# Performance work log

Hardware: AMD Instinct MI355X
Metric: run time of the kernel (lower is better)

The kernel has to match this reference:

```python
import jax, jax.numpy as jnp
import numpy as np

ROUTING_ITERS = 3


def _squash(x, axis=-1):
    # sum_sq/(1+sum_sq) * x/sqrt(sum_sq), faithful to the torch squash
    sum_sq = jnp.sum(x * x, axis=axis, keepdims=True)
    return sum_sq / (1.0 + sum_sq) * x / jnp.sqrt(sum_sq)


def setup_inputs() -> dict:
    key = jax.random.key(0)
    k1, k2 = jax.random.split(key)
    B, I, O, Din, Dout = 256, 1152, 10, 8, 16
    x = jax.random.normal(k1, (B, I, Din), dtype=jnp.float32)
    W = jax.random.normal(k2, (I, O, Din, Dout), dtype=jnp.float32)
    return {"x": x, "W": W}


def reference(x, W):
    # x: [B, I, Din], W: [I, O, Din, Dout]
    I, O, Din, Dout = W.shape
    # u_hat = x @ W per (capsule_in, capsule_out): [B, I, O, Dout]
    u_hat = jnp.einsum('bid,iode->bioe', x, W)
    b = jnp.zeros((I, O), dtype=x.dtype)  # coupling logits, shared over batch
    v = None
    for _ in range(ROUTING_ITERS):
        c = jax.nn.softmax(b, axis=1)                    # softmax over out capsules
        s = jnp.einsum('bioe,io->boe', u_hat, c)         # weighted sum over in caps
        v = _squash(s, axis=-1)                          # [B, O, Dout]
        # agreement, averaged over batch (torch does .mean(dim=0))
        agree = jnp.einsum('bioe,boe->bio', u_hat, v).mean(axis=0)  # [I, O]
        b = b + agree
    # torch returns v.squeeze(1).transpose(2,3) -> [B, O, Dout, 1]
    return v[..., None]
```

## Files before the change

### kernel.cpp

```cpp
#include <hip/hip_runtime.h>
#include <math.h>

#define B    256
#define I    1152
#define O    10
#define DIN  8
#define DOUT 16
#define OE   160
#define XROW 9216
#define WROW 1280
#define PSPLIT 72
#define CHUNK  16
#define SI     8

typedef __attribute__((ext_vector_type(8))) short short8;
typedef __attribute__((ext_vector_type(4))) float floatx4;

__device__ __forceinline__ unsigned short f2bf(float f) {
    unsigned u = __builtin_bit_cast(unsigned, f);
    u += 0x7fffu + ((u >> 16) & 1u);
    return (unsigned short)(u >> 16);
}
__device__ __forceinline__ float bf2f(unsigned short h) {
    unsigned u = ((unsigned)h) << 16;
    return __builtin_bit_cast(float, u);
}

__global__ __launch_bounds__(256) void xsplit_kernel(
    const float* __restrict__ x,
    unsigned short* __restrict__ xh, unsigned short* __restrict__ xl)
{
    int g = blockIdx.x * 256 + threadIdx.x;
    float4 v = ((const float4*)x)[g];
    ushort4 h, l;
    h.x = f2bf(v.x); l.x = f2bf(v.x - bf2f(h.x));
    h.y = f2bf(v.y); l.y = f2bf(v.y - bf2f(h.y));
    h.z = f2bf(v.z); l.z = f2bf(v.z - bf2f(h.z));
    h.w = f2bf(v.w); l.w = f2bf(v.w - bf2f(h.w));
    ((ushort4*)xh)[g] = h;
    ((ushort4*)xl)[g] = l;
}

__global__ __launch_bounds__(256) void spart_mfma(
    const unsigned short* __restrict__ xh, const unsigned short* __restrict__ xl,
    const float* __restrict__ W, const float* __restrict__ c,
    float* __restrict__ sp, int first)
{
    __shared__ unsigned short Wh[80 * 64], Wl[80 * 64];
    __shared__ unsigned short Xh[128 * 64], Xl[128 * 64];

    int bid = blockIdx.x;
    int ic  = bid >> 2;
    int mb  = (bid >> 1) & 1;
    int nb  = bid & 1;
    int b0  = mb * 128;
    int oe0 = nb * 80;
    int o0  = nb * 5;
    int i0  = ic * CHUNK;

    int t    = threadIdx.x;
    int w    = t >> 6;
    int lane = t & 63;
    int l15  = lane & 15;
    int q    = lane >> 4;

    floatx4 acc[2][5];
#pragma unroll
    for (int mt = 0; mt < 2; ++mt)
#pragma unroll
        for (int nt = 0; nt < 5; ++nt) acc[mt][nt] = (floatx4)(0.f);

#pragma unroll
    for (int round = 0; round < CHUNK / SI; ++round) {
        int si0 = i0 + round * SI;
        if (round) __syncthreads();

#pragma unroll
        for (int r = 0; r < 3; ++r) {
            int p = t + 256 * r;
            if (p < 640) {
                int oeL = p % 80;
                int iL  = p / 80;
                int o   = o0 + (oeL >> 4);
                int e   = oeL & 15;
                const float* wp = W + (size_t)(si0 + iL) * WROW + o * (DIN * DOUT) + e;
                float cv = first ? 0.1f : c[(si0 + iL) * O + o];
                short8 hv, lv;
#pragma unroll
                for (int d = 0; d < 8; ++d) {
                    float wv = wp[d * DOUT] * cv;
                    unsigned short h = f2bf(wv);
                    hv[d] = (short)h;
                    lv[d] = (short)f2bf(wv - bf2f(h));
                }
                int off = oeL * 64 + ((iL ^ (oeL & 7)) << 3);
                *(short8*)(Wh + off) = hv;
                *(short8*)(Wl + off) = lv;
            }
        }
#pragma unroll
        for (int r = 0; r < 4; ++r) {
            int cg  = t + 256 * r;
            int row = cg >> 3;
            int ch  = cg & 7;
            size_t goff = (size_t)(b0 + row) * XROW + (size_t)si0 * 8 + (ch << 3);
            short8 vh = *(const short8*)(xh + goff);
            short8 vl = *(const short8*)(xl + goff);
            int off = row * 64 + ((ch ^ (row & 7)) << 3);
            *(short8*)(Xh + off) = vh;
            *(short8*)(Xl + off) = vl;
        }
        __syncthreads();

#pragma unroll
        for (int ks = 0; ks < 2; ++ks) {
            short8 ah[2], al[2];
#pragma unroll
            for (int mt = 0; mt < 2; ++mt) {
                int rm  = w * 32 + mt * 16 + l15;
                int off = rm * 64 + ((((ks << 2) + q) ^ (rm & 7)) << 3);
                ah[mt] = *(const short8*)(Xh + off);
                al[mt] = *(const short8*)(Xl + off);
            }
#pragma unroll
            for (int nt = 0; nt < 5; ++nt) {
                int rn  = nt * 16 + l15;
                int off = rn * 64 + ((((ks << 2) + q) ^ (rn & 7)) << 3);
                short8 bh = *(const short8*)(Wh + off);
                short8 bl = *(const short8*)(Wl + off);
#pragma unroll
                for (int mt = 0; mt < 2; ++mt) {
                    acc[mt][nt] = __builtin_amdgcn_mfma_f32_16x16x32_bf16(ah[mt], bh, acc[mt][nt], 0, 0, 0);
                    acc[mt][nt] = __builtin_amdgcn_mfma_f32_16x16x32_bf16(ah[mt], bl, acc[mt][nt], 0, 0, 0);
                    acc[mt][nt] = __builtin_amdgcn_mfma_f32_16x16x32_bf16(al[mt], bh, acc[mt][nt], 0, 0, 0);
                }
            }
        }
    }

    float* base = sp + (size_t)ic * (B * OE);
#pragma unroll
    for (int mt = 0; mt < 2; ++mt) {
        int row0 = b0 + w * 32 + mt * 16 + q * 4;
#pragma unroll
        for (int nt = 0; nt < 5; ++nt) {
            int col = oe0 + nt * 16 + l15;
#pragma unroll
            for (int reg = 0; reg < 4; ++reg)
                base[(row0 + reg) * OE + col] = acc[mt][nt][reg];
        }
    }
}

__global__ __launch_bounds__(256) void vred_kernel(
    const float* __restrict__ sp, float* __restrict__ dst)
{
    int g = blockIdx.x * 256 + threadIdx.x;
    float s = 0.f;
#pragma unroll 4
    for (int ic = 0; ic < PSPLIT; ++ic) s += sp[(size_t)ic * (B * OE) + g];

    float ss = s * s;
    ss += __shfl_xor(ss, 1, 16);
    ss += __shfl_xor(ss, 2, 16);
    ss += __shfl_xor(ss, 4, 16);
    ss += __shfl_xor(ss, 8, 16);
    float f = sqrtf(ss) / (1.f + ss);
    dst[g] = s * f;
}

__global__ __launch_bounds__(320) void agree_kernel(
    const float* __restrict__ x, const float* __restrict__ W,
    const float* __restrict__ v, float* __restrict__ blog,
    float* __restrict__ c, int first)
{
    int i  = blockIdx.x;
    int t  = threadIdx.x;
    int dg = (t >= OE) ? 1 : 0;
    int oe = t - dg * OE;

    __shared__ float4 Xl[B][2];
    __shared__ float  G[DIN * OE];
    __shared__ float  brow[O];

#pragma unroll
    for (int k = 0; k < 2; ++k) {
        int idx = t + 320 * k;
        if (idx < 512) {
            int r = idx >> 1;
            int h = idx & 1;
            Xl[r][h] = *(const float4*)(x + (size_t)r * XROW + i * DIN + h * 4);
        }
    }
    __syncthreads();

    float a0 = 0.f, a1 = 0.f, a2 = 0.f, a3 = 0.f;
    const float* vp = v + oe;
#pragma unroll 8
    for (int bb = 0; bb < B; ++bb) {
        float  vv = vp[bb * OE];
        float4 xq = Xl[bb][dg];
        a0 = fmaf(xq.x, vv, a0);
        a1 = fmaf(xq.y, vv, a1);
        a2 = fmaf(xq.z, vv, a2);
        a3 = fmaf(xq.w, vv, a3);
    }

    int d0 = dg * 4;
    G[(d0 + 0) * OE + oe] = a0;
    G[(d0 + 1) * OE + oe] = a1;
    G[(d0 + 2) * OE + oe] = a2;
    G[(d0 + 3) * OE + oe] = a3;
    __syncthreads();

    if (t < OE) {
        int o = t >> 4;
        const float* wr = W + (size_t)i * WROW + o * (DIN * DOUT) + (t & 15);
        float p = 0.f;
#pragma unroll
        for (int d = 0; d < DIN; ++d) p = fmaf(wr[d * DOUT], G[d * OE + t], p);
        p += __shfl_xor(p, 8, 16);
        p += __shfl_xor(p, 4, 16);
        p += __shfl_xor(p, 2, 16);
        p += __shfl_xor(p, 1, 16);
        if ((t & 15) == 0) {
            float bo = first ? 0.f : blog[i * O + o];
            bo += p * (1.f / (float)B);
            blog[i * O + o] = bo;
            brow[o] = bo;
        }
    }
    __syncthreads();

    if (t == 0) {
        float m = brow[0];
#pragma unroll
        for (int o = 1; o < O; ++o) m = fmaxf(m, brow[o]);
        float ex[O];
        float sum = 0.f;
#pragma unroll
        for (int o = 0; o < O; ++o) { ex[o] = __expf(brow[o] - m); sum += ex[o]; }
        float inv = 1.f / sum;
#pragma unroll
        for (int o = 0; o < O; ++o) c[i * O + o] = ex[o] * inv;
    }
}

extern "C" void kernel_launch(void* const* d_in, const int* in_sizes, int n_in,
                              void* d_out, int out_size, void* d_ws, size_t ws_size,
                              hipStream_t stream)
{
    const float* x = (const float*)d_in[0];
    const float* W = (const float*)d_in[1];
    float* out = (float*)d_out;

    unsigned short* xh = (unsigned short*)d_ws;
    unsigned short* xl = xh + (size_t)B * XROW;
    float* blog = (float*)(xl + (size_t)B * XROW);
    float* cbuf = blog + I * O;
    float* vbuf = cbuf + I * O;
    float* sp   = vbuf + B * OE;

    xsplit_kernel<<<(B * XROW) / (256 * 4), 256, 0, stream>>>(x, xh, xl);

    dim3 gs(4 * PSPLIT), bs(256);
    spart_mfma<<<gs, bs, 0, stream>>>(xh, xl, W, cbuf, sp, 1);
    vred_kernel<<<160, 256, 0, stream>>>(sp, vbuf);
    agree_kernel<<<I, 320, 0, stream>>>(x, W, vbuf, blog, cbuf, 1);
    spart_mfma<<<gs, bs, 0, stream>>>(xh, xl, W, cbuf, sp, 0);
    vred_kernel<<<160, 256, 0, stream>>>(sp, vbuf);
    agree_kernel<<<I, 320, 0, stream>>>(x, W, vbuf, blog, cbuf, 0);
    spart_mfma<<<gs, bs, 0, stream>>>(xh, xl, W, cbuf, sp, 0);
    vred_kernel<<<160, 256, 0, stream>>>(sp, out);
}
```

Baseline: 164.5 us.

## Fuse all routing stages into one persistent kernel with grid barriers

Result: slower. 645.2 us (+292.3%).

```diff
diff --git a/kernel.cpp b/kernel.cpp
--- a/kernel.cpp
+++ b/kernel.cpp
@@ -2,16 +2,16 @@
 #include <math.h>
 
 #define B    256
-#define I    1152
+#define I_   1152
 #define O    10
 #define DIN  8
-#define DOUT 16
 #define OE   160
 #define XROW 9216
 #define WROW 1280
 #define PSPLIT 72
 #define CHUNK  16
-#define SI     8
+#define LROW   40
+#define NBLK   256
 
 typedef __attribute__((ext_vector_type(8))) short short8;
 typedef __attribute__((ext_vector_type(4))) float floatx4;
@@ -25,224 +25,224 @@
     unsigned u = ((unsigned)h) << 16;
     return __builtin_bit_cast(float, u);
 }
-
-__global__ __launch_bounds__(256) void xsplit_kernel(
-    const float* __restrict__ x,
-    unsigned short* __restrict__ xh, unsigned short* __restrict__ xl)
+__device__ __forceinline__ void split8(const float* s, short8& hv, short8& lv) {
+#pragma unroll
+    for (int d = 0; d < 8; ++d) {
+        unsigned short h = f2bf(s[d]);
+        hv[d] = (short)h;
+        lv[d] = (short)f2bf(s[d] - bf2f(h));
+    }
+}
+
+__device__ __forceinline__ void grid_bar(int* cnt, int* gen) {
+    __syncthreads();
+    if (threadIdx.x == 0) {
+        __threadfence();
+        int g = __hip_atomic_load(gen, __ATOMIC_RELAXED, __HIP_MEMORY_SCOPE_AGENT);
+        int prev = __hip_atomic_fetch_add(cnt, 1, __ATOMIC_ACQ_REL, __HIP_MEMORY_SCOPE_AGENT);
+        if (prev == NBLK - 1) {
+            __hip_atomic_store(cnt, 0, __ATOMIC_RELAXED, __HIP_MEMORY_SCOPE_AGENT);
+            __hip_atomic_fetch_add(gen, 1, __ATOMIC_RELEASE, __HIP_MEMORY_SCOPE_AGENT);
+        } else {
+            while (__hip_atomic_load(gen, __ATOMIC_RELAXED, __HIP_MEMORY_SCOPE_AGENT) == g)
+                __builtin_amdgcn_s_sleep(2);
+        }
+        __threadfence();
+    }
+    __syncthreads();
+}
+
+template<int NI>
+__device__ __forceinline__ void agree_phase(
+    const float* __restrict__ x, const float* __restrict__ W,
+    const float* __restrict__ v, float* __restrict__ cbuf,
+    float* bl, float (*brow)[16], int iStart, int t)
 {
-    int g = blockIdx.x * 256 + threadIdx.x;
-    float4 v = ((const float4*)x)[g];
-    ushort4 h, l;
-    h.x = f2bf(v.x); l.x = f2bf(v.x - bf2f(h.x));
-    h.y = f2bf(v.y); l.y = f2bf(v.y - bf2f(h.y));
-    h.z = f2bf(v.z); l.z = f2bf(v.z - bf2f(h.z));
-    h.w = f2bf(v.w); l.w = f2bf(v.w - bf2f(h.w));
-    ((ushort4*)xh)[g] = h;
-    ((ushort4*)xl)[g] = l;
-}
-
-__global__ __launch_bounds__(256) void spart_mfma(
-    const unsigned short* __restrict__ xh, const unsigned short* __restrict__ xl,
-    const float* __restrict__ W, const float* __restrict__ c,
-    float* __restrict__ sp, int first)
+    const int o = t >> 4, e = t & 15;
+    if (t < OE) {
+        float acc[NI][8];
+#pragma unroll
+        for (int ii = 0; ii < NI; ++ii)
+#pragma unroll
+            for (int d = 0; d < 8; ++d) acc[ii][d] = 0.f;
+
+#pragma unroll 4
+        for (int b = 0; b < B; ++b) {
+            float vv = v[b * OE + t];
+            const float* xr = x + (size_t)b * XROW + iStart * DIN;
+#pragma unroll
+            for (int ii = 0; ii < NI; ++ii)
+#pragma unroll
+                for (int d = 0; d < 8; ++d)
+                    acc[ii][d] = fmaf(xr[ii * 8 + d], vv, acc[ii][d]);
+        }
+#pragma unroll
+        for (int ii = 0; ii < NI; ++ii) {
+            const float* wr = W + (size_t)(iStart + ii) * WROW + o * 128 + e;
+            float p = 0.f;
+#pragma unroll
+            for (int d = 0; d < 8; ++d) p = fmaf(wr[d * 16], acc[ii][d], p);
+            p += __shfl_xor(p, 8, 16);
+            p += __shfl_xor(p, 4, 16);
+            p += __shfl_xor(p, 2, 16);
+            p += __shfl_xor(p, 1, 16);
+            bl[ii] += p * (1.f / 256.f);
+            if (e == 0) brow[ii][o] = bl[ii];
+        }
+    }
+    __syncthreads();
+    if (t < NI) {
+        float m = brow[t][0];
+#pragma unroll
+        for (int oo = 1; oo < O; ++oo) m = fmaxf(m, brow[t][oo]);
+        float ex[O], sum = 0.f;
+#pragma unroll
+        for (int oo = 0; oo < O; ++oo) { ex[oo] = __expf(brow[t][oo] - m); sum += ex[oo]; }
+        float inv = 1.f / sum;
+#pragma unroll
+        for (int oo = 0; oo < O; ++oo) cbuf[(iStart + t) * O + oo] = ex[oo] * inv;
+    }
+}
+
+__global__ void __launch_bounds__(256)
+capsnet_fused(const float* __restrict__ x, const float* __restrict__ W,
+              float* __restrict__ out,
+              unsigned short* __restrict__ xh, unsigned short* __restrict__ xl,
+              float* __restrict__ cbuf, float* __restrict__ vbuf,
+              float* __restrict__ sp, int* __restrict__ bar)
 {
-    __shared__ unsigned short Wh[80 * 64], Wl[80 * 64];
-    __shared__ unsigned short Xh[128 * 64], Xl[128 * 64];
-
-    int bid = blockIdx.x;
-    int ic  = bid >> 2;
-    int mb  = (bid >> 1) & 1;
-    int nb  = bid & 1;
-    int b0  = mb * 128;
-    int oe0 = nb * 80;
-    int o0  = nb * 5;
-    int i0  = ic * CHUNK;
-
-    int t    = threadIdx.x;
-    int w    = t >> 6;
-    int lane = t & 63;
-    int l15  = lane & 15;
-    int q    = lane >> 4;
-
-    floatx4 acc[2][5];
-#pragma unroll
-    for (int mt = 0; mt < 2; ++mt)
-#pragma unroll
-        for (int nt = 0; nt < 5; ++nt) acc[mt][nt] = (floatx4)(0.f);
-
-#pragma unroll
-    for (int round = 0; round < CHUNK / SI; ++round) {
-        int si0 = i0 + round * SI;
-        if (round) __syncthreads();
-
-#pragma unroll
-        for (int r = 0; r < 3; ++r) {
-            int p = t + 256 * r;
-            if (p < 640) {
-                int oeL = p % 80;
-                int iL  = p / 80;
-                int o   = o0 + (oeL >> 4);
-                int e   = oeL & 15;
-                const float* wp = W + (size_t)(si0 + iL) * WROW + o * (DIN * DOUT) + e;
-                float cv = first ? 0.1f : c[(si0 + iL) * O + o];
-                short8 hv, lv;
-#pragma unroll
-                for (int d = 0; d < 8; ++d) {
-                    float wv = wp[d * DOUT] * cv;
-                    unsigned short h = f2bf(wv);
-                    hv[d] = (short)h;
-                    lv[d] = (short)f2bf(wv - bf2f(h));
-                }
-                int off = oeL * 64 + ((iL ^ (oeL & 7)) << 3);
-                *(short8*)(Wh + off) = hv;
-                *(short8*)(Wl + off) = lv;
+    __shared__ unsigned short sWh[OE * LROW], sWl[OE * LROW];
+    __shared__ unsigned short sXh[128 * LROW], sXl[128 * LROW];
+    __shared__ float sBrow[5][16];
+
+    int* bcnt = bar;
+    int* bgen = bar + 16;
+
+    const int blk = blockIdx.x;
+    const int t   = threadIdx.x;
+
+    float bl[5] = {0.f, 0.f, 0.f, 0.f, 0.f};
+    int iStart, ni;
+    if (blk < 128) { ni = 5; iStart = blk * 5; }
+    else           { ni = 4; iStart = 640 + (blk - 128) * 4; }
+
+    for (int iter = 0; iter < 3; ++iter) {
+        const int first = (iter == 0);
+
+        if (blk < 144) {
+            const int ic = blk >> 1;
+            const int mb = blk & 1;
+            const int b0 = mb * 128;
+            const int i0 = ic * CHUNK;
+            const int w = t >> 6, lane = t & 63, l15 = lane & 15, q = lane >> 4;
+
+            floatx4 acc[2][10];
+#pragma unroll
+            for (int mt = 0; mt < 2; ++mt)
+#pragma unroll
+                for (int nt = 0; nt < 10; ++nt) acc[mt][nt] = (floatx4)(0.f);
+
+            for (int round = 0; round < 4; ++round) {
+                const int si0 = i0 + round * 4;
+                if (round) __syncthreads();
+
+#pragma unroll
+                for (int r = 0; r < 3; ++r) {
+                    int p = t + 256 * r;
+                    if (p < 640) {
+                        int oeL = p % 160;
+                        int iL  = p / 160;
+                        int o = oeL >> 4, e = oeL & 15;
+                        const float* wp = W + (size_t)(si0 + iL) * WROW + o * 128 + e;
+                        float cv = first ? 0.1f : cbuf[(si0 + iL) * O + o];
+                        float tmp[8];
+#pragma unroll
+                        for (int d = 0; d < 8; ++d) tmp[d] = wp[d * 16] * cv;
+                        short8 hv, lv; split8(tmp, hv, lv);
+                        int off = oeL * LROW + iL * 8;
+                        *(short8*)(sWh + off) = hv;
+                        *(short8*)(sWl + off) = lv;
+                    }
+                }
+#pragma unroll
+                for (int r = 0; r < 2; ++r) {
+                    int cgi = t + 256 * r;
+                    int row = cgi >> 2, ch = cgi & 3;
+                    size_t goff = (size_t)(b0 + row) * XROW + (size_t)si0 * 8 + ch * 8;
+                    short8 hv, lv;
+                    if (first) {
+                        float tmp[8];
+#pragma unroll
+                        for (int d = 0; d < 8; ++d) tmp[d] = x[goff + d];
+                        split8(tmp, hv, lv);
+                        *(short8*)(xh + goff) = hv;
+                        *(short8*)(xl + goff) = lv;
+                    } else {
+                        hv = *(const short8*)(xh + goff);
+                        lv = *(const short8*)(xl + goff);
+                    }
+                    int off = row * LROW + ch * 8;
+                    *(short8*)(sXh + off) = hv;
+                    *(short8*)(sXl + off) = lv;
+                }
+                __syncthreads();
+
+                short8 ah[2], al[2];
+#pragma unroll
+                for (int mt = 0; mt < 2; ++mt) {
+                    int rm = w * 32 + mt * 16 + l15;
+                    int off = rm * LROW + q * 8;
+                    ah[mt] = *(const short8*)(sXh + off);
+                    al[mt] = *(const short8*)(sXl + off);
+                }
+#pragma unroll
+                for (int nt = 0; nt < 10; ++nt) {
+                    int rn = nt * 16 + l15;
+                    int off = rn * LROW + q * 8;
+                    short8 bh = *(const short8*)(sWh + off);
+                    short8 bv = *(const short8*)(sWl + off);
+#pragma unroll
+                    for (int mt = 0; mt < 2; ++mt) {
+                        acc[mt][nt] = __builtin_amdgcn_mfma_f32_16x16x32_bf16(ah[mt], bh, acc[mt][nt], 0, 0, 0);
+                        acc[mt][nt] = __builtin_amdgcn_mfma_f32_16x16x32_bf16(ah[mt], bv, acc[mt][nt], 0, 0, 0);
+                        acc[mt][nt] = __builtin_amdgcn_mfma_f32_16x16x32_bf16(al[mt], bh, acc[mt][nt], 0, 0, 0);
+                    }
+                }
             }
-        }
-#pragma unroll
-        for (int r = 0; r < 4; ++r) {
-            int cg  = t + 256 * r;
-            int row = cg >> 3;
-            int ch  = cg & 7;
-            size_t goff = (size_t)(b0 + row) * XROW + (size_t)si0 * 8 + (ch << 3);
-            short8 vh = *(const short8*)(xh + goff);
-            short8 vl = *(const short8*)(xl + goff);
-            int off = row * 64 + ((ch ^ (row & 7)) << 3);
-            *(short8*)(Xh + off) = vh;
-            *(short8*)(Xl + off) = vl;
-        }
-        __syncthreads();
-
-#pragma unroll
-        for (int ks = 0; ks < 2; ++ks) {
-            short8 ah[2], al[2];
+            float* base = sp + (size_t)ic * (B * OE);
 #pragma unroll
             for (int mt = 0; mt < 2; ++mt) {
-                int rm  = w * 32 + mt * 16 + l15;
-                int off = rm * 64 + ((((ks << 2) + q) ^ (rm & 7)) << 3);
-                ah[mt] = *(const short8*)(Xh + off);
-                al[mt] = *(const short8*)(Xl + off);
+                int row0 = b0 + w * 32 + mt * 16 + q * 4;
+#pragma unroll
+                for (int nt = 0; nt < 10; ++nt) {
+                    int col = nt * 16 + l15;
+#pragma unroll
+                    for (int reg = 0; reg < 4; ++reg)
+                        base[(size_t)(row0 + reg) * OE + col] = acc[mt][nt][reg];
+                }
             }
-#pragma unroll
-            for (int nt = 0; nt < 5; ++nt) {
-                int rn  = nt * 16 + l15;
-                int off = rn * 64 + ((((ks << 2) + q) ^ (rn & 7)) << 3);
-                short8 bh = *(const short8*)(Wh + off);
-                short8 bl = *(const short8*)(Wl + off);
-#pragma unroll
-                for (int mt = 0; mt < 2; ++mt) {
-                    acc[mt][nt] = __builtin_amdgcn_mfma_f32_16x16x32_bf16(ah[mt], bh, acc[mt][nt], 0, 0, 0);
-                    acc[mt][nt] = __builtin_amdgcn_mfma_f32_16x16x32_bf16(ah[mt], bl, acc[mt][nt], 0, 0, 0);
-                    acc[mt][nt] = __builtin_amdgcn_mfma_f32_16x16x32_bf16(al[mt], bh, acc[mt][nt], 0, 0, 0);
-                }
-            }
-        }
-    }
-
-    float* base = sp + (size_t)ic * (B * OE);
-#pragma unroll
-    for (int mt = 0; mt < 2; ++mt) {
-        int row0 = b0 + w * 32 + mt * 16 + q * 4;
-#pragma unroll
-        for (int nt = 0; nt < 5; ++nt) {
-            int col = oe0 + nt * 16 + l15;
-#pragma unroll
-            for (int reg = 0; reg < 4; ++reg)
-                base[(row0 + reg) * OE + col] = acc[mt][nt][reg];
-        }
-    }
-}
-
-__global__ __launch_bounds__(256) void vred_kernel(
-    const float* __restrict__ sp, float* __restrict__ dst)
-{
-    int g = blockIdx.x * 256 + threadIdx.x;
-    float s = 0.f;
-#pragma unroll 4
-    for (int ic = 0; ic < PSPLIT; ++ic) s += sp[(size_t)ic * (B * OE) + g];
-
-    float ss = s * s;
-    ss += __shfl_xor(ss, 1, 16);
-    ss += __shfl_xor(ss, 2, 16);
-    ss += __shfl_xor(ss, 4, 16);
-    ss += __shfl_xor(ss, 8, 16);
-    float f = sqrtf(ss) / (1.f + ss);
-    dst[g] = s * f;
-}
-
-__global__ __launch_bounds__(320) void agree_kernel(
-    const float* __restrict__ x, const float* __restrict__ W,
-    const float* __restrict__ v, float* __restrict__ blog,
-    float* __restrict__ c, int first)
-{
-    int i  = blockIdx.x;
-    int t  = threadIdx.x;
-    int dg = (t >= OE) ? 1 : 0;
-    int oe = t - dg * OE;
-
-    __shared__ float4 Xl[B][2];
-    __shared__ float  G[DIN * OE];
-    __shared__ float  brow[O];
-
-#pragma unroll
-    for (int k = 0; k < 2; ++k) {
-        int idx = t + 320 * k;
-        if (idx < 512) {
-            int r = idx >> 1;
-            int h = idx & 1;
-            Xl[r][h] = *(const float4*)(x + (size_t)r * XROW + i * DIN + h * 4);
-        }
-    }
-    __syncthreads();
-
-    float a0 = 0.f, a1 = 0.f, a2 = 0.f, a3 = 0.f;
-    const float* vp = v + oe;
+        }
+        grid_bar(bcnt, bgen);
+
+        if (blk < 160) {
+            float* dst = (iter == 2) ? out : vbuf;
+            int g = blk * 256 + t;
+            float s = 0.f;
 #pragma unroll 8
-    for (int bb = 0; bb < B; ++bb) {
-        float  vv = vp[bb * OE];
-        float4 xq = Xl[bb][dg];
-        a0 = fmaf(xq.x, vv, a0);
-        a1 = fmaf(xq.y, vv, a1);
-        a2 = fmaf(xq.z, vv, a2);
-        a3 = fmaf(xq.w, vv, a3);
-    }
-
-    int d0 = dg * 4;
-    G[(d0 + 0) * OE + oe] = a0;
-    G[(d0 + 1) * OE + oe] = a1;
-    G[(d0 + 2) * OE + oe] = a2;
-    G[(d0 + 3) * OE + oe] = a3;
-    __syncthreads();
-
-    if (t < OE) {
-        int o = t >> 4;
-        const float* wr = W + (size_t)i * WROW + o * (DIN * DOUT) + (t & 15);
-        float p = 0.f;
-#pragma unroll
-        for (int d = 0; d < DIN; ++d) p = fmaf(wr[d * DOUT], G[d * OE + t], p);
-        p += __shfl_xor(p, 8, 16);
-        p += __shfl_xor(p, 4, 16);
-        p += __shfl_xor(p, 2, 16);
-        p += __shfl_xor(p, 1, 16);
-        if ((t & 15) == 0) {
-            float bo = first ? 0.f : blog[i * O + o];
-            bo += p * (1.f / (float)B);
-            blog[i * O + o] = bo;
-            brow[o] = bo;
-        }
-    }
-    __syncthreads();
-
-    if (t == 0) {
-        float m = brow[0];
-#pragma unroll
-        for (int o = 1; o < O; ++o) m = fmaxf(m, brow[o]);
-        float ex[O];
-        float sum = 0.f;
-#pragma unroll
-        for (int o = 0; o < O; ++o) { ex[o] = __expf(brow[o] - m); sum += ex[o]; }
-        float inv = 1.f / sum;
-#pragma unroll
-        for (int o = 0; o < O; ++o) c[i * O + o] = ex[o] * inv;
+            for (int icc = 0; icc < PSPLIT; ++icc) s += sp[(size_t)icc * (B * OE) + g];
+            float ss = s * s;
+            ss += __shfl_xor(ss, 1, 16);
+            ss += __shfl_xor(ss, 2, 16);
+            ss += __shfl_xor(ss, 4, 16);
+            ss += __shfl_xor(ss, 8, 16);
+            dst[g] = s * (sqrtf(ss) / (1.f + ss));
+        }
+        if (iter == 2) break;
+        grid_bar(bcnt, bgen);
+
+        if (ni == 5) agree_phase<5>(x, W, vbuf, cbuf, bl, sBrow, iStart, t);
+        else         agree_phase<4>(x, W, vbuf, cbuf, bl, sBrow, iStart, t);
+        grid_bar(bcnt, bgen);
     }
 }
 
@@ -254,22 +254,15 @@
     const float* W = (const float*)d_in[1];
     float* out = (float*)d_out;
 
-    unsigned short* xh = (unsigned short*)d_ws;
+    int* bar = (int*)d_ws;
+    unsigned short* xh = (unsigned short*)((char*)d_ws + 256);
     unsigned short* xl = xh + (size_t)B * XROW;
-    float* blog = (float*)(xl + (size_t)B * XROW);
-    float* cbuf = blog + I * O;
-    float* vbuf = cbuf + I * O;
+    float* cbuf = (float*)(xl + (size_t)B * XROW);
+    float* vbuf = cbuf + I_ * O;
     float* sp   = vbuf + B * OE;
 
-    xsplit_kernel<<<(B * XROW) / (256 * 4), 256, 0, stream>>>(x, xh, xl);
-
-    dim3 gs(4 * PSPLIT), bs(256);
-    spart_mfma<<<gs, bs, 0, stream>>>(xh, xl, W, cbuf, sp, 1);
-    vred_kernel<<<160, 256, 0, stream>>>(sp, vbuf);
-    agree_kernel<<<I, 320, 0, stream>>>(x, W, vbuf, blog, cbuf, 1);
-    spart_mfma<<<gs, bs, 0, stream>>>(xh, xl, W, cbuf, sp, 0);
-    vred_kernel<<<160, 256, 0, stream>>>(sp, vbuf);
-    agree_kernel<<<I, 320, 0, stream>>>(x, W, vbuf, blog, cbuf, 0);
-    spart_mfma<<<gs, bs, 0, stream>>>(xh, xl, W, cbuf, sp, 0);
-    vred_kernel<<<160, 256, 0, stream>>>(sp, out);
-}
+    hipMemsetAsync(bar, 0, 256, stream);
+
+    capsnet_fused<<<dim3(NBLK), dim3(256), 0, stream>>>(
+        x, W, out, xh, xl, cbuf, vbuf, sp, bar);
+}
```
